# Performance work log

Hardware: AMD Instinct MI355X
Metric: run time of the kernel (lower is better)

## Reference

```python
import jax, jax.numpy as jnp
import numpy as np

BATCH = 131072
S = 128  # state_size == x_size


def setup_inputs() -> dict:
    key = jax.random.key(0)
    ks = jax.random.split(key, 7)
    std = 1.0 / np.sqrt(S).astype(np.float32)
    return {
        "x": jax.random.normal(ks[0], (BATCH, S), dtype=jnp.float32),
        "old_h": jax.random.normal(ks[1], (BATCH, S), dtype=jnp.float32),
        "W_x1": jax.random.normal(ks[2], (3, S, S), dtype=jnp.float32) * std,
        "W_x2": jax.random.normal(ks[3], (3, S, S), dtype=jnp.float32) * std,
        "W_h": jax.random.normal(ks[4], (6, S, S), dtype=jnp.float32) * std,
        "b": jnp.zeros((6, 1, S), dtype=jnp.float32),
        "mid": jax.random.normal(ks[5], (S, S), dtype=jnp.float32) * std,
    }


def reference(x, old_h, W_x1, W_x2, W_h, b, mid):
    sg = jax.nn.sigmoid
    # --- first GRU stage ---
    z = sg(x @ W_x1[0] + old_h @ W_h[0] + b[0])
    r = sg(x @ W_x1[1] + old_h @ W_h[1] + b[1])
    h_tilde = jnp.tanh(x @ W_x1[2] + (r * old_h) @ W_h[2] + b[2])
    mid_h = z * old_h + (1.0 - z) * h_tilde
    # mid_dropout with p=0 is identity
    mid_x = jax.nn.relu(mid_h @ mid)
    # --- second GRU stage (faithfully reuses W_h[0], b[0] as in source) ---
    z2 = sg(mid_x @ W_x2[0] + mid_h @ W_h[0] + b[0])
    r2 = sg(mid_x @ W_x2[1] + mid_h @ W_h[4] + b[4])
    h2_tilde = jnp.tanh(mid_x @ W_x2[2] + (r2 * mid_h) @ W_h[5] + b[5])
    h = z2 * mid_h + (1.0 - z2) * h2_tilde
    return (h,)
```

## Files before the change

### kernel.cpp

```cpp
#include <hip/hip_runtime.h>
#include <hip/hip_bf16.h>
#include <cstdint>


typedef __attribute__((ext_vector_type(8))) short bf16x8;
typedef __attribute__((ext_vector_type(4))) float f32x4;

#define S 128
#define BM 64
#define THREADS 512

#define SWZB(row) (((((row) & 7) ^ (((row) >> 2) & 2))) << 4)

__device__ __forceinline__ unsigned short f2bf(float f) {
    __hip_bfloat16 h = __float2bfloat16(f);
    return *reinterpret_cast<unsigned short*>(&h);
}
__device__ __forceinline__ float bf2f(unsigned short h) {
    unsigned int u = ((unsigned int)h) << 16;
    return __builtin_bit_cast(float, u);
}

__device__ __forceinline__ float fast_sig(float t) {
    float e = __expf(-t);
    return __builtin_amdgcn_rcpf(1.0f + e);
}
__device__ __forceinline__ float fast_tanh(float t) {
    float e = __expf(-2.0f * t);
    return __builtin_fmaf(2.0f, __builtin_amdgcn_rcpf(1.0f + e), -1.0f);
}

__global__ void pack_weights(const float* __restrict__ wx1,
                             const float* __restrict__ wx2,
                             const float* __restrict__ wh,
                             const float* __restrict__ mid,
                             unsigned short* __restrict__ dst) {
    int mat = blockIdx.x;
    const float* src;
    if (mat < 3)       src = wx1 + mat * (S * S);
    else if (mat < 6)  src = wx2 + (mat - 3) * (S * S);
    else if (mat < 12) src = wh  + (mat - 6) * (S * S);
    else               src = mid;
    int t = threadIdx.x;
    for (int f8 = 0; f8 < 8; ++f8) {
        int slot = f8 * 256 + t;
        int frag = slot >> 6;
        int lane = slot & 63;
        int kt  = frag >> 3;
        int ntg = frag & 7;
        int k0  = kt * 32 + (lane >> 4) * 8;
        int col = ntg * 16 + (lane & 15);
        unsigned int w[4];
#pragma unroll
        for (int p = 0; p < 4; ++p) {
            unsigned int lo = f2bf(src[(k0 + 2 * p) * S + col]);
            unsigned int hi = f2bf(src[(k0 + 2 * p + 1) * S + col]);
            w[p] = lo | (hi << 16);
        }
        uint4* d = (uint4*)(dst + (size_t)mat * (S * S) + frag * 512 + lane * 8);
        *d = make_uint4(w[0], w[1], w[2], w[3]);
    }
}

__device__ __forceinline__ bf16x8 lds_afrag(const unsigned short* s, int row, int kt, int lane) {
    int byte = row * 256 + kt * 64 + ((lane >> 4) << 4);
    byte ^= SWZB(row);
    return *(const bf16x8*)((const char*)s + byte);
}
__device__ __forceinline__ void st_bf(unsigned short* s, int row, int col, float v) {
    int byte = (row * 256 + col * 2) ^ SWZB(row);
    *(unsigned short*)((char*)s + byte) = f2bf(v);
}
__device__ __forceinline__ float ld_bf(const unsigned short* s, int row, int col) {
    int byte = (row * 256 + col * 2) ^ SWZB(row);
    return bf2f(*(const unsigned short*)((const char*)s + byte));
}

__device__ __forceinline__ void gemm_single(f32x4 (&acc)[4],
        const unsigned short* sA,
        const unsigned short* __restrict__ w0,
        int lane, int wc) {
    int rbase = lane & 15;
    __builtin_amdgcn_s_setprio(1);
#pragma unroll
    for (int kt = 0; kt < 4; ++kt) {
        bf16x8 a0[4];
#pragma unroll
        for (int m = 0; m < 4; ++m)
            a0[m] = lds_afrag(sA, rbase + m * 16, kt, lane);
        bf16x8 b0 = *(const bf16x8*)(w0 + (kt * 8 + wc) * 512 + lane * 8);
#pragma unroll
        for (int m = 0; m < 4; ++m)
            acc[m] = __builtin_amdgcn_mfma_f32_16x16x32_bf16(a0[m], b0, acc[m], 0, 0, 0);
    }
    __builtin_amdgcn_s_setprio(0);
}

__device__ __forceinline__ void gemm_pair2(f32x4 (&acc0)[4], f32x4 (&acc1)[4],
        const unsigned short* sA,
        const unsigned short* __restrict__ w0,
        const unsigned short* __restrict__ w1,
        int lane, int wc) {
    int rbase = lane & 15;
    __builtin_amdgcn_s_setprio(1);
#pragma unroll
    for (int kt = 0; kt < 4; ++kt) {
        bf16x8 a0[4];
#pragma unroll
        for (int m = 0; m < 4; ++m)
            a0[m] = lds_afrag(sA, rbase + m * 16, kt, lane);
        bf16x8 b0 = *(const bf16x8*)(w0 + (kt * 8 + wc) * 512 + lane * 8);
        bf16x8 b1 = *(const bf16x8*)(w1 + (kt * 8 + wc) * 512 + lane * 8);
#pragma unroll
        for (int m = 0; m < 4; ++m) {
            acc0[m] = __builtin_amdgcn_mfma_f32_16x16x32_bf16(a0[m], b0, acc0[m], 0, 0, 0);
            acc1[m] = __builtin_amdgcn_mfma_f32_16x16x32_bf16(a0[m], b1, acc1[m], 0, 0, 0);
        }
    }
    __builtin_amdgcn_s_setprio(0);
}

template <int OP>
__device__ __forceinline__ void finish(f32x4 (&acc)[4], float bc) {
#pragma unroll
    for (int m = 0; m < 4; ++m)
#pragma unroll
        for (int i = 0; i < 4; ++i) {
            float t = acc[m][i] + bc;
            acc[m][i] = (OP == 0) ? fast_sig(t) : fast_tanh(t);
        }
}

#define ZERO_ACC(A)                                           \
    _Pragma("unroll") for (int m = 0; m < 4; ++m)             \
        A[m] = (f32x4){0.f, 0.f, 0.f, 0.f};

#define FOR_COORDS(BODY)                                      \
    _Pragma("unroll") for (int m = 0; m < 4; ++m)             \
    _Pragma("unroll") for (int i = 0; i < 4; ++i) {           \
        int rt  = m * 16 + ((lane >> 4) << 2) + i;            \
        int col = wc * 16 + (lane & 15);                      \
        BODY                                                  \
    }

__global__ __launch_bounds__(THREADS, 4)
void dgru_main(const float* __restrict__ x, const float* __restrict__ old_h,
               const float* __restrict__ b, const unsigned short* __restrict__ wpk,
               float* __restrict__ out) {
    __shared__ __align__(16) unsigned short sx[S * BM];
    __shared__ __align__(16) unsigned short sh[S * BM];
    __shared__ __align__(16) unsigned short sg[S * BM];

    const int tid  = threadIdx.x;
    const int lane = tid & 63;
    const int wc   = tid >> 6;
    const long row0 = (long)blockIdx.x * BM;

    float bld[6];
#pragma unroll
    for (int j = 0; j < 6; ++j)
        bld[j] = b[j * S + wc * 16 + (lane & 15)];

#pragma unroll
    for (int it = 0; it < 2; ++it) {
        int slot = it * THREADS + tid;
        int row  = slot >> 4;
        int c8   = slot & 15;
        const float4* px = (const float4*)(x     + (row0 + row) * S + c8 * 8);
        const float4* ph = (const float4*)(old_h + (row0 + row) * S + c8 * 8);
        float4 v0 = px[0], v1 = px[1];
        float4 u0 = ph[0], u1 = ph[1];
        int byte = (row * 256 + c8 * 16) ^ SWZB(row);
        uint4 wx, wh;
        wx.x = (unsigned)f2bf(v0.x) | ((unsigned)f2bf(v0.y) << 16);
        wx.y = (unsigned)f2bf(v0.z) | ((unsigned)f2bf(v0.w) << 16);
        wx.z = (unsigned)f2bf(v1.x) | ((unsigned)f2bf(v1.y) << 16);
        wx.w = (unsigned)f2bf(v1.z) | ((unsigned)f2bf(v1.w) << 16);
        wh.x = (unsigned)f2bf(u0.x) | ((unsigned)f2bf(u0.y) << 16);
        wh.y = (unsigned)f2bf(u0.z) | ((unsigned)f2bf(u0.w) << 16);
        wh.z = (unsigned)f2bf(u1.x) | ((unsigned)f2bf(u1.y) << 16);
        wh.w = (unsigned)f2bf(u1.z) | ((unsigned)f2bf(u1.w) << 16);
        *(uint4*)((char*)sx + byte) = wx;
        *(uint4*)((char*)sh + byte) = wh;
    }
    __syncthreads();

#define WP(m) (wpk + (size_t)(m) * (S * S))

    f32x4 zz[4]; ZERO_ACC(zz);
    {
        f32x4 rr[4]; ZERO_ACC(rr);
        gemm_pair2(zz, rr, sx, WP(0), WP(1), lane, wc);
        gemm_pair2(zz, rr, sh, WP(6), WP(7), lane, wc);
        finish<0>(zz, bld[0]);
        finish<0>(rr, bld[1]);
        FOR_COORDS({
            float oh = ld_bf(sh, rt, col);
            st_bf(sg, rt, col, rr[m][i] * oh);
        })
    }
    __syncthreads();

    {
        f32x4 ht[4]; ZERO_ACC(ht);
        gemm_single(ht, sx, WP(2), lane, wc);
        gemm_single(ht, sg, WP(8), lane, wc);
        finish<1>(ht, bld[2]);
        FOR_COORDS({
            float oh = ld_bf(sh, rt, col);
            float z  = zz[m][i];
            st_bf(sh, rt, col, z * oh + (1.0f - z) * ht[m][i]);
        })
    }
    __syncthreads();

    {
        f32x4 mx[4]; ZERO_ACC(mx);
        gemm_single(mx, sh, WP(12), lane, wc);
        FOR_COORDS({
            float v = mx[m][i];
            st_bf(sx, rt, col, v > 0.0f ? v : 0.0f);
        })
    }
    __syncthreads();

    f32x4 z2[4]; ZERO_ACC(z2);
    {
        f32x4 r2[4]; ZERO_ACC(r2);
        gemm_pair2(z2, r2, sx, WP(3), WP(4), lane, wc);
        gemm_pair2(z2, r2, sh, WP(6), WP(10), lane, wc);
        finish<0>(z2, bld[0]);
        finish<0>(r2, bld[4]);
        FOR_COORDS({
            float mhv = ld_bf(sh, rt, col);
            st_bf(sg, rt, col, r2[m][i] * mhv);
        })
    }
    __syncthreads();

    {
        f32x4 h2[4]; ZERO_ACC(h2);
        gemm_single(h2, sx, WP(5), lane, wc);
        gemm_single(h2, sg, WP(11), lane, wc);
        finish<1>(h2, bld[5]);
        FOR_COORDS({
            float z   = z2[m][i];
            float mhv = ld_bf(sh, rt, col);
            h2[m][i] = z * mhv + (1.0f - z) * h2[m][i];
        })
        __syncthreads();
        FOR_COORDS({ st_bf(sg, rt, col, h2[m][i]); })
    }
    __syncthreads();

#pragma unroll
    for (int it = 0; it < 2; ++it) {
        int slot = it * THREADS + tid;
        int row  = slot >> 4;
        int c8   = slot & 15;
        int byte = (row * 256 + c8 * 16) ^ SWZB(row);
        bf16x8 v = *(const bf16x8*)((const char*)sg + byte);
        float4 f0, f1;
        f0.x = bf2f((unsigned short)v[0]); f0.y = bf2f((unsigned short)v[1]);
        f0.z = bf2f((unsigned short)v[2]); f0.w = bf2f((unsigned short)v[3]);
        f1.x = bf2f((unsigned short)v[4]); f1.y = bf2f((unsigned short)v[5]);
        f1.z = bf2f((unsigned short)v[6]); f1.w = bf2f((unsigned short)v[7]);
        float4* po = (float4*)(out + (row0 + row) * S + c8 * 8);
        po[0] = f0;
        po[1] = f1;
    }
}

extern "C" void kernel_launch(void* const* d_in, const int* in_sizes, int n_in,
                              void* d_out, int out_size, void* d_ws, size_t ws_size,
                              hipStream_t stream) {
    const float* x     = (const float*)d_in[0];
    const float* old_h = (const float*)d_in[1];
    const float* W_x1  = (const float*)d_in[2];
    const float* W_x2  = (const float*)d_in[3];
    const float* W_h   = (const float*)d_in[4];
    const float* b     = (const float*)d_in[5];
    const float* mid   = (const float*)d_in[6];
    float* out = (float*)d_out;
    unsigned short* wpk = (unsigned short*)d_ws;

    int batch = in_sizes[0] / S;

    pack_weights<<<13, 256, 0, stream>>>(W_x1, W_x2, W_h, mid, wpk);
    dgru_main<<<batch / BM, THREADS, 0, stream>>>(x, old_h, b, wpk, out);
}
```

Measured before the change: 99.38 us.

## Process four row tiles per block and prefetch next tile during last GEMM

Each block now loops over four 64-row tiles instead of one. It issues global loads for the next tile's x and old_h before the final GEMM stage, then writes them into shared memory afterwards, so memory latency overlaps compute. A separate output LDS buffer lets the next tile's inputs land without clobbering the result being written out. This adds 16KB of shared memory per block, which may cut occupancy, and the grid shrinks by four times, which may hurt load balance.

Measured after the change: 316.6 us. 3.19x slower.

```diff
diff --git a/kernel.cpp b/kernel.cpp
--- a/kernel.cpp
+++ b/kernel.cpp
@@ -8,6 +8,7 @@
 
 #define S 128
 #define BM 64
+#define TPB 4
 #define THREADS 512
 
 #define SWZB(row) (((((row) & 7) ^ (((row) >> 2) & 2))) << 4)
@@ -75,6 +76,16 @@
     int byte = (row * 256 + col * 2) ^ SWZB(row);
     return bf2f(*(const unsigned short*)((const char*)s + byte));
 }
+__device__ __forceinline__ void st_row8(unsigned short* s, int row, int c8,
+                                        float4 a, float4 bq) {
+    int byte = (row * 256 + c8 * 16) ^ SWZB(row);
+    uint4 w;
+    w.x = (unsigned)f2bf(a.x)  | ((unsigned)f2bf(a.y)  << 16);
+    w.y = (unsigned)f2bf(a.z)  | ((unsigned)f2bf(a.w)  << 16);
+    w.z = (unsigned)f2bf(bq.x) | ((unsigned)f2bf(bq.y) << 16);
+    w.w = (unsigned)f2bf(bq.z) | ((unsigned)f2bf(bq.w) << 16);
+    *(uint4*)((char*)s + byte) = w;
+}
 
 __device__ __forceinline__ void gemm_single(f32x4 (&acc)[4],
         const unsigned short* sA,
@@ -150,11 +161,12 @@
     __shared__ __align__(16) unsigned short sx[S * BM];
     __shared__ __align__(16) unsigned short sh[S * BM];
     __shared__ __align__(16) unsigned short sg[S * BM];
+    __shared__ __align__(16) unsigned short so[S * BM];
 
     const int tid  = threadIdx.x;
     const int lane = tid & 63;
     const int wc   = tid >> 6;
-    const long row0 = (long)blockIdx.x * BM;
+    const long base0 = (long)blockIdx.x * (BM * TPB);
 
     float bld[6];
 #pragma unroll
@@ -166,108 +178,126 @@
         int slot = it * THREADS + tid;
         int row  = slot >> 4;
         int c8   = slot & 15;
-        const float4* px = (const float4*)(x     + (row0 + row) * S + c8 * 8);
-        const float4* ph = (const float4*)(old_h + (row0 + row) * S + c8 * 8);
-        float4 v0 = px[0], v1 = px[1];
-        float4 u0 = ph[0], u1 = ph[1];
-        int byte = (row * 256 + c8 * 16) ^ SWZB(row);
-        uint4 wx, wh;
-        wx.x = (unsigned)f2bf(v0.x) | ((unsigned)f2bf(v0.y) << 16);
-        wx.y = (unsigned)f2bf(v0.z) | ((unsigned)f2bf(v0.w) << 16);
-        wx.z = (unsigned)f2bf(v1.x) | ((unsigned)f2bf(v1.y) << 16);
-        wx.w = (unsigned)f2bf(v1.z) | ((unsigned)f2bf(v1.w) << 16);
-        wh.x = (unsigned)f2bf(u0.x) | ((unsigned)f2bf(u0.y) << 16);
-        wh.y = (unsigned)f2bf(u0.z) | ((unsigned)f2bf(u0.w) << 16);
-        wh.z = (unsigned)f2bf(u1.x) | ((unsigned)f2bf(u1.y) << 16);
-        wh.w = (unsigned)f2bf(u1.z) | ((unsigned)f2bf(u1.w) << 16);
-        *(uint4*)((char*)sx + byte) = wx;
-        *(uint4*)((char*)sh + byte) = wh;
+        const float4* px = (const float4*)(x     + (base0 + row) * S + c8 * 8);
+        const float4* ph = (const float4*)(old_h + (base0 + row) * S + c8 * 8);
+        st_row8(sx, row, c8, px[0], px[1]);
+        st_row8(sh, row, c8, ph[0], ph[1]);
     }
     __syncthreads();
 
 #define WP(m) (wpk + (size_t)(m) * (S * S))
 
-    f32x4 zz[4]; ZERO_ACC(zz);
-    {
-        f32x4 rr[4]; ZERO_ACC(rr);
-        gemm_pair2(zz, rr, sx, WP(0), WP(1), lane, wc);
-        gemm_pair2(zz, rr, sh, WP(6), WP(7), lane, wc);
-        finish<0>(zz, bld[0]);
-        finish<0>(rr, bld[1]);
-        FOR_COORDS({
-            float oh = ld_bf(sh, rt, col);
-            st_bf(sg, rt, col, rr[m][i] * oh);
-        })
-    }
-    __syncthreads();
-
-    {
-        f32x4 ht[4]; ZERO_ACC(ht);
-        gemm_single(ht, sx, WP(2), lane, wc);
-        gemm_single(ht, sg, WP(8), lane, wc);
-        finish<1>(ht, bld[2]);
-        FOR_COORDS({
-            float oh = ld_bf(sh, rt, col);
-            float z  = zz[m][i];
-            st_bf(sh, rt, col, z * oh + (1.0f - z) * ht[m][i]);
-        })
-    }
-    __syncthreads();
-
-    {
-        f32x4 mx[4]; ZERO_ACC(mx);
-        gemm_single(mx, sh, WP(12), lane, wc);
-        FOR_COORDS({
-            float v = mx[m][i];
-            st_bf(sx, rt, col, v > 0.0f ? v : 0.0f);
-        })
-    }
-    __syncthreads();
-
-    f32x4 z2[4]; ZERO_ACC(z2);
-    {
-        f32x4 r2[4]; ZERO_ACC(r2);
-        gemm_pair2(z2, r2, sx, WP(3), WP(4), lane, wc);
-        gemm_pair2(z2, r2, sh, WP(6), WP(10), lane, wc);
-        finish<0>(z2, bld[0]);
-        finish<0>(r2, bld[4]);
-        FOR_COORDS({
-            float mhv = ld_bf(sh, rt, col);
-            st_bf(sg, rt, col, r2[m][i] * mhv);
-        })
-    }
-    __syncthreads();
-
-    {
-        f32x4 h2[4]; ZERO_ACC(h2);
-        gemm_single(h2, sx, WP(5), lane, wc);
-        gemm_single(h2, sg, WP(11), lane, wc);
-        finish<1>(h2, bld[5]);
-        FOR_COORDS({
-            float z   = z2[m][i];
-            float mhv = ld_bf(sh, rt, col);
-            h2[m][i] = z * mhv + (1.0f - z) * h2[m][i];
-        })
-        __syncthreads();
-        FOR_COORDS({ st_bf(sg, rt, col, h2[m][i]); })
-    }
-    __syncthreads();
-
-#pragma unroll
-    for (int it = 0; it < 2; ++it) {
-        int slot = it * THREADS + tid;
-        int row  = slot >> 4;
-        int c8   = slot & 15;
-        int byte = (row * 256 + c8 * 16) ^ SWZB(row);
-        bf16x8 v = *(const bf16x8*)((const char*)sg + byte);
-        float4 f0, f1;
-        f0.x = bf2f((unsigned short)v[0]); f0.y = bf2f((unsigned short)v[1]);
-        f0.z = bf2f((unsigned short)v[2]); f0.w = bf2f((unsigned short)v[3]);
-        f1.x = bf2f((unsigned short)v[4]); f1.y = bf2f((unsigned short)v[5]);
-        f1.z = bf2f((unsigned short)v[6]); f1.w = bf2f((unsigned short)v[7]);
-        float4* po = (float4*)(out + (row0 + row) * S + c8 * 8);
-        po[0] = f0;
-        po[1] = f1;
+    for (int t = 0; t < TPB; ++t) {
+        const long row0 = base0 + (long)t * BM;
+
+        f32x4 zz[4]; ZERO_ACC(zz);
+        {
+            f32x4 rr[4]; ZERO_ACC(rr);
+            gemm_pair2(zz, rr, sx, WP(0), WP(1), lane, wc);
+            gemm_pair2(zz, rr, sh, WP(6), WP(7), lane, wc);
+            finish<0>(zz, bld[0]);
+            finish<0>(rr, bld[1]);
+            FOR_COORDS({
+                float oh = ld_bf(sh, rt, col);
+                st_bf(sg, rt, col, rr[m][i] * oh);
+            })
+        }
+        __syncthreads();
+
+        {
+            f32x4 ht[4]; ZERO_ACC(ht);
+            gemm_single(ht, sx, WP(2), lane, wc);
+            gemm_single(ht, sg, WP(8), lane, wc);
+            finish<1>(ht, bld[2]);
+            FOR_COORDS({
+                float oh = ld_bf(sh, rt, col);
+                float z  = zz[m][i];
+                st_bf(sh, rt, col, z * oh + (1.0f - z) * ht[m][i]);
+            })
+        }
+        __syncthreads();
+
+        {
+            f32x4 mx[4]; ZERO_ACC(mx);
+            gemm_single(mx, sh, WP(12), lane, wc);
+            FOR_COORDS({
+                float v = mx[m][i];
+                st_bf(sx, rt, col, v > 0.0f ? v : 0.0f);
+            })
+        }
+        __syncthreads();
+
+        f32x4 z2[4]; ZERO_ACC(z2);
+        {
+            f32x4 r2[4]; ZERO_ACC(r2);
+            gemm_pair2(z2, r2, sx, WP(3), WP(4), lane, wc);
+            gemm_pair2(z2, r2, sh, WP(6), WP(10), lane, wc);
+            finish<0>(z2, bld[0]);
+            finish<0>(r2, bld[4]);
+            FOR_COORDS({
+                float mhv = ld_bf(sh, rt, col);
+                st_bf(sg, rt, col, r2[m][i] * mhv);
+            })
+        }
+        __syncthreads();
+
+        {
+            float4 nx[2][2], nh[2][2];
+            const bool have_next = (t + 1 < TPB);
+            if (have_next) {
+                const long r0n = row0 + BM;
+#pragma unroll
+                for (int it = 0; it < 2; ++it) {
+                    int slot = it * THREADS + tid;
+                    int row  = slot >> 4;
+                    int c8   = slot & 15;
+                    const float4* px = (const float4*)(x     + (r0n + row) * S + c8 * 8);
+                    const float4* ph = (const float4*)(old_h + (r0n + row) * S + c8 * 8);
+                    nx[it][0] = px[0]; nx[it][1] = px[1];
+                    nh[it][0] = ph[0]; nh[it][1] = ph[1];
+                }
+            }
+
+            f32x4 h2[4]; ZERO_ACC(h2);
+            gemm_single(h2, sx, WP(5), lane, wc);
+            gemm_single(h2, sg, WP(11), lane, wc);
+            finish<1>(h2, bld[5]);
+            FOR_COORDS({
+                float z   = z2[m][i];
+                float mhv = ld_bf(sh, rt, col);
+                h2[m][i] = z * mhv + (1.0f - z) * h2[m][i];
+            })
+            __syncthreads();
+            FOR_COORDS({ st_bf(so, rt, col, h2[m][i]); })
+            if (have_next) {
+#pragma unroll
+                for (int it = 0; it < 2; ++it) {
+                    int slot = it * THREADS + tid;
+                    int row  = slot >> 4;
+                    int c8   = slot & 15;
+                    st_row8(sx, row, c8, nx[it][0], nx[it][1]);
+                    st_row8(sh, row, c8, nh[it][0], nh[it][1]);
+                }
+            }
+        }
+        __syncthreads();
+
+#pragma unroll
+        for (int it = 0; it < 2; ++it) {
+            int slot = it * THREADS + tid;
+            int row  = slot >> 4;
+            int c8   = slot & 15;
+            int byte = (row * 256 + c8 * 16) ^ SWZB(row);
+            bf16x8 v = *(const bf16x8*)((const char*)so + byte);
+            float4 f0, f1;
+            f0.x = bf2f((unsigned short)v[0]); f0.y = bf2f((unsigned short)v[1]);
+            f0.z = bf2f((unsigned short)v[2]); f0.w = bf2f((unsigned short)v[3]);
+            f1.x = bf2f((unsigned short)v[4]); f1.y = bf2f((unsigned short)v[5]);
+            f1.z = bf2f((unsigned short)v[6]); f1.w = bf2f((unsigned short)v[7]);
+            float4* po = (float4*)(out + (row0 + row) * S + c8 * 8);
+            po[0] = f0;
+            po[1] = f1;
+        }
     }
 }
 
@@ -287,5 +317,5 @@
     int batch = in_sizes[0] / S;
 
     pack_weights<<<13, 256, 0, stream>>>(W_x1, W_x2, W_h, mid, wpk);
-    dgru_main<<<batch / BM, THREADS, 0, stream>>>(x, old_h, b, wpk, out);
-}
+    dgru_main<<<batch / (BM * TPB), THREADS, 0, stream>>>(x, old_h, b, wpk, out);
+}
```
